# Kernel optimization log

Hardware: AMD Instinct MI355X
Metric: run time of the kernel (lower is better)

The kernel has to match this reference:

```python
import jax, jax.numpy as jnp
import numpy as np
from jax import lax

SEQ, FEAT, U1, U2, U3, OUT = 20, 5, 10, 7, 4, 4
BATCH = 262144


def _he_uniform(key, shape, fan_in):
    lim = np.sqrt(6.0 / fan_in)
    return jax.random.uniform(key, shape, jnp.float32, -lim, lim)


def _orthogonal(key, n, m):
    a = jax.random.normal(key, (max(n, m), min(n, m)), jnp.float32)
    q, _ = jnp.linalg.qr(a)
    return q[:n, :m] if n >= m else q[:m, :n].T


def _lstm_params(key, in_dim, units):
    k1, k2 = jax.random.split(key)
    Wk = _he_uniform(k1, (in_dim, 4 * units), in_dim)
    Wr = _orthogonal(k2, units, 4 * units)
    # Keras unit_forget_bias: bias = [zeros(i), ones(f), zeros(c), zeros(o)]
    b = jnp.concatenate([jnp.zeros(units), jnp.ones(units), jnp.zeros(2 * units)]).astype(jnp.float32)
    return Wk, Wr, b


def setup_inputs() -> dict:
    key = jax.random.key(0)
    ks = jax.random.split(key, 5)
    x = jax.random.normal(ks[0], (BATCH, SEQ, FEAT), jnp.float32)
    Wk1, Wr1, b1 = _lstm_params(ks[1], FEAT, U1)
    Wk2, Wr2, b2 = _lstm_params(ks[2], U1, U2)
    Wk3, Wr3, b3 = _lstm_params(ks[3], U2, U3)
    kd1, kd2 = jax.random.split(ks[4])
    lim = np.sqrt(6.0 / (U3 + OUT))  # glorot_uniform (Dense default)
    Wd = jax.random.uniform(kd1, (U3, OUT), jnp.float32, -lim, lim)
    bd = jnp.zeros((OUT,), jnp.float32)
    return {"x": x, "Wk1": Wk1, "Wr1": Wr1, "b1": b1,
            "Wk2": Wk2, "Wr2": Wr2, "b2": b2,
            "Wk3": Wk3, "Wr3": Wr3, "b3": b3,
            "Wd": Wd, "bd": bd}


def lstm_layer(x, Wk, Wr, b):
    # x: [B, T, F] -> h-sequence [B, T, U]; Keras gate order i, f, c(g), o
    B = x.shape[0]
    U = Wr.shape[0]
    # precompute input projection for all timesteps (one big GEMM)
    zx = jnp.einsum('btf,fg->btg', x, Wk) + b  # [B, T, 4U]
    zxT = jnp.swapaxes(zx, 0, 1)               # [T, B, 4U]

    def step(carry, zt):
        h, c = carry
        z = zt + h @ Wr
        i, f, g, o = jnp.split(z, 4, axis=-1)
        i = jax.nn.sigmoid(i)
        f = jax.nn.sigmoid(f)
        g = jnp.tanh(g)
        o = jax.nn.sigmoid(o)
        c = f * c + i * g
        h = o * jnp.tanh(c)
        return (h, c), h

    init = (jnp.zeros((B, U), x.dtype), jnp.zeros((B, U), x.dtype))
    _, hs = lax.scan(step, init, zxT)
    return jnp.swapaxes(hs, 0, 1)  # [B, T, U]


def reference(x, Wk1, Wr1, b1, Wk2, Wr2, b2, Wk3, Wr3, b3, Wd, bd):
    h = lstm_layer(x, Wk1, Wr1, b1)
    h = lstm_layer(h, Wk2, Wr2, b2)
    h = lstm_layer(h, Wk3, Wr3, b3)
    return jax.nn.sigmoid(jnp.einsum('btu,uo->bto', h, Wd) + bd)
```

## Files before the change

### kernel.cpp

```cpp
#include <hip/hip_runtime.h>

static constexpr int SEQ = 20, FEAT = 5, NU1 = 10, NU2 = 7, NU3 = 4, NOUT = 4;

typedef short bf16x8 __attribute__((ext_vector_type(8)));
typedef float f32x4  __attribute__((ext_vector_type(4)));


__device__ __forceinline__ unsigned short bf16_hi_rne(float x) {
    unsigned u = __float_as_uint(x);
    return (unsigned short)((u + 0x7FFF + ((u >> 16) & 1)) >> 16);
}
__device__ __forceinline__ unsigned short bf16_trunc(float x) {
    return (unsigned short)(__float_as_uint(x) >> 16);
}
__device__ __forceinline__ float bf16_to_f(unsigned short h) {
    return __uint_as_float(((unsigned)h) << 16);
}
__device__ __forceinline__ unsigned hpack(float h) {
    unsigned rp;
    asm("v_cvt_pk_bf16_f32 %0, %1, %1" : "=v"(rp) : "v"(h));
    float lo = h - __uint_as_float(rp << 16);
    return __builtin_amdgcn_perm(__float_as_uint(lo), rp, 0x07060100u);
}

__device__ __forceinline__ float sigm(float x) {
    return __builtin_amdgcn_rcpf(1.0f + __builtin_amdgcn_exp2f(x * -1.4426950408889634f));
}
__device__ __forceinline__ float ftanh(float x) {
    return 1.0f - 2.0f * __builtin_amdgcn_rcpf(1.0f + __builtin_amdgcn_exp2f(x * 2.8853900817779268f));
}

__device__ __forceinline__ unsigned act_unit(const f32x4 z, float& c) {
    float gi = sigm(z[0]), gf = sigm(z[1]), gg = ftanh(z[2]), go = sigm(z[3]);
    c = gf * c + gi * gg;
    return hpack(go * ftanh(c));
}

__device__ __forceinline__ unsigned bperm(int idx, unsigned v) {
    return (unsigned)__builtin_amdgcn_ds_bpermute(idx, (int)v);
}
__device__ __forceinline__ bf16x8 bfrag(unsigned v0, unsigned v1) {
    uint4 u{v0, v0, v1, v1};
    return __builtin_bit_cast(bf16x8, u);
}

__global__ void build_afrags(const float* Wk1, const float* Wr1, const float* b1,
                             const float* Wk2, const float* Wr2, const float* b2,
                             const float* Wk3, const float* Wr3, const float* b3,
                             const float* Wd,  const float* bd, unsigned* ws) {
    const int lane = threadIdx.x;
    const int m = lane & 15;
    const int qh = lane >> 4;

    for (int tau = 0; tau < 3; ++tau)
    for (int kap = 0; kap < 2; ++kap) {
        unsigned short h8[8];
        for (int j = 0; j < 8; ++j) {
            const int k = kap * 32 + qh * 8 + j;
            const int i = k >> 2, cls = k & 3;
            const int u = tau * 4 + (m >> 2), col = (m & 3) * NU1 + u;
            unsigned short v = 0;
            if (u < NU1) {
                if (i < 15) {
                    float W;
                    if (i < 8)       W = Wr1[((i >> 1) + 4 * (i & 1)) * 40 + col];
                    else if (i < 10) W = Wr1[i * 40 + col];
                    else             W = Wk1[(i - 10) * 40 + col];
                    unsigned short hi = bf16_hi_rne(W);
                    v = (cls < 2) ? hi : bf16_trunc(W - bf16_to_f(hi));
                } else if (i == 15) {
                    float bv = b1[col];
                    unsigned short hi = bf16_hi_rne(bv);
                    v = (cls == 0) ? hi : ((cls == 1) ? bf16_trunc(bv - bf16_to_f(hi)) : (unsigned short)0);
                }
            }
            h8[j] = v;
        }
        const int id = tau * 2 + kap;
        for (int d = 0; d < 4; ++d)
            ws[id * 256 + lane * 4 + d] = (unsigned)h8[2 * d] | ((unsigned)h8[2 * d + 1] << 16);
    }
    for (int tau = 0; tau < 2; ++tau)
    for (int kap = 0; kap < 3; ++kap) {
        unsigned short h8[8];
        for (int j = 0; j < 8; ++j) {
            const int k = kap * 32 + qh * 8 + j;
            const int i = k >> 2, cls = k & 3;
            const int u = tau * 4 + (m >> 2), col = (m & 3) * NU2 + u;
            unsigned short v = 0;
            if (u < NU2) {
                if (i < 17) {
                    float W;
                    if (i < 8)        W = Wk2[((i >> 1) + 4 * (i & 1)) * 28 + col];
                    else if (i < 10)  W = Wk2[i * 28 + col];
                    else if (i < 16)  W = Wr2[(((i - 10) >> 1) + 4 * ((i - 10) & 1)) * 28 + col];
                    else              W = Wr2[3 * 28 + col];
                    unsigned short hi = bf16_hi_rne(W);
                    v = (cls < 2) ? hi : bf16_trunc(W - bf16_to_f(hi));
                } else if (i == 17) {
                    float bv = b2[col];
                    unsigned short hi = bf16_hi_rne(bv);
                    v = (cls == 0) ? hi : ((cls == 1) ? bf16_trunc(bv - bf16_to_f(hi)) : (unsigned short)0);
                }
            }
            h8[j] = v;
        }
        const int id = 6 + tau * 3 + kap;
        for (int d = 0; d < 4; ++d)
            ws[id * 256 + lane * 4 + d] = (unsigned)h8[2 * d] | ((unsigned)h8[2 * d + 1] << 16);
    }
    for (int kap = 0; kap < 2; ++kap) {
        unsigned short h8[8];
        for (int j = 0; j < 8; ++j) {
            const int k = kap * 32 + qh * 8 + j;
            const int i = k >> 2, cls = k & 3;
            const int u = m >> 2, col = (m & 3) * NU3 + u;
            unsigned short v = 0;
            if (i < 11) {
                float W;
                if (i < 6)       W = Wk3[((i >> 1) + 4 * (i & 1)) * 16 + col];
                else if (i == 6) W = Wk3[3 * 16 + col];
                else             W = Wr3[(i - 7) * 16 + col];
                unsigned short hi = bf16_hi_rne(W);
                v = (cls < 2) ? hi : bf16_trunc(W - bf16_to_f(hi));
            } else if (i == 11) {
                float bv = b3[col];
                unsigned short hi = bf16_hi_rne(bv);
                v = (cls == 0) ? hi : ((cls == 1) ? bf16_trunc(bv - bf16_to_f(hi)) : (unsigned short)0);
            }
            h8[j] = v;
        }
        const int id = 12 + kap;
        for (int d = 0; d < 4; ++d)
            ws[id * 256 + lane * 4 + d] = (unsigned)h8[2 * d] | ((unsigned)h8[2 * d + 1] << 16);
    }
    {
        unsigned short h8[8];
        for (int j = 0; j < 8; ++j) {
            const int k = qh * 8 + j;
            const int i = k >> 2, cls = k & 3;
            unsigned short v = 0;
            if (m < NOUT) {
                if (i < 4) {
                    float W = Wd[i * NOUT + m];
                    unsigned short hi = bf16_hi_rne(W);
                    v = (cls < 2) ? hi : bf16_trunc(W - bf16_to_f(hi));
                } else if (i == 4) {
                    float bv = bd[m];
                    unsigned short hi = bf16_hi_rne(bv);
                    v = (cls == 0) ? hi : ((cls == 1) ? bf16_trunc(bv - bf16_to_f(hi)) : (unsigned short)0);
                }
            }
            h8[j] = v;
        }
        for (int d = 0; d < 4; ++d)
            ws[14 * 256 + lane * 4 + d] = (unsigned)h8[2 * d] | ((unsigned)h8[2 * d + 1] << 16);
    }
}

__global__ __launch_bounds__(256, 4) void lstm3_mfma(
    const float* __restrict__ x, const unsigned* __restrict__ wsA,
    float* __restrict__ out, int B) {
    const int tid = threadIdx.x;
    const int lane = tid & 63;
    const int n = lane & 15;
    const int q = lane >> 4;

    bf16x8 af[15];
#pragma unroll
    for (int i = 0; i < 15; ++i) {
        uint4 v = ((const uint4*)wsA)[i * 64 + lane];
        af[i] = __builtin_bit_cast(bf16x8, v);
    }

    const int i_h19 = (n + 16) << 2;
    const int i_sh  = (n + 16 * ((q + 3) & 3)) << 2;
    const int i_r1  = (n + 16 * ((q + 1) & 3)) << 2;
    const int i_r2  = (n + 16 * ((q + 2) & 3)) << 2;

    const unsigned ONE = 0x3F803F80u;
    const f32x4 zro = {0.f, 0.f, 0.f, 0.f};

    const int ngrp = B >> 4;
    const int gw = (blockIdx.x * blockDim.x + tid) >> 6;
    const int nw = (gridDim.x * blockDim.x) >> 6;

    for (int grp = gw; grp < ngrp; grp += nw) {
        const float* xr = x + (size_t)grp * 16 * (SEQ * FEAT) + n * (SEQ * FEAT);
        float* ob = out + (size_t)grp * 16 * (SEQ * NOUT) + n * (SEQ * NOUT);

        unsigned p1a = 0, p1b = 0, p1c = 0, t9 = 0;
        unsigned p2a = 0, p2b = 0, p3 = 0, rot = 0, rot2 = 0;
        float c10 = 0.f, c11 = 0.f, c12 = 0.f, c20 = 0.f, c21 = 0.f, c30 = 0.f;

        float xa = 0.f, xc = 0.f;
        if (q != 0) {
            const float* p = xr + 2 * (q - 1);
            xa = p[0];
            if (q != 3) xc = p[1];
        }

#pragma unroll 1
        for (int t = 0; t < SEQ; ++t) {
            const unsigned xP0 = hpack(xa), xP1 = hpack(xc);
            {
                const int tn = (t + 1 < SEQ) ? t + 1 : 0;
                if (q != 0) {
                    const float* p = xr + tn * FEAT + 2 * (q - 1);
                    xa = p[0];
                    if (q != 3) xc = p[1];
                }
            }
            bf16x8 bF0 = bfrag(p1a, p1b);
            unsigned F1v0 = (q == 0) ? p1c : xP0;
            unsigned F1v1 = (q == 0) ? t9 : ((q == 3) ? ONE : xP1);
            bf16x8 bF1 = bfrag(F1v0, F1v1);
            f32x4 z0 = __builtin_amdgcn_mfma_f32_16x16x32_bf16(af[0], bF0, zro, 0, 0, 0);
            z0 = __builtin_amdgcn_mfma_f32_16x16x32_bf16(af[1], bF1, z0, 0, 0, 0);
            f32x4 z1 = __builtin_amdgcn_mfma_f32_16x16x32_bf16(af[2], bF0, zro, 0, 0, 0);
            z1 = __builtin_amdgcn_mfma_f32_16x16x32_bf16(af[3], bF1, z1, 0, 0, 0);
            f32x4 z2 = __builtin_amdgcn_mfma_f32_16x16x32_bf16(af[4], bF0, zro, 0, 0, 0);
            z2 = __builtin_amdgcn_mfma_f32_16x16x32_bf16(af[5], bF1, z2, 0, 0, 0);
            const unsigned s2a = bperm(i_sh, p2a);
            const unsigned s2b = bperm(i_sh, p2b);
            p1a = act_unit(z0, c10);
            p1b = act_unit(z1, c11);
            p1c = act_unit(z2, c12);
            t9  = bperm(i_h19, p1c);
            bf16x8 bA  = bfrag(p1a, p1b);
            unsigned F2v0 = (q == 0) ? p1c : s2a;
            unsigned F2v1 = (q == 0) ? t9  : s2b;
            bf16x8 bF2 = bfrag(F2v0, F2v1);
            bf16x8 bF3 = bfrag(s2a, ONE);
            f32x4 y0 = __builtin_amdgcn_mfma_f32_16x16x32_bf16(af[6], bA, zro, 0, 0, 0);
            y0 = __builtin_amdgcn_mfma_f32_16x16x32_bf16(af[7], bF2, y0, 0, 0, 0);
            y0 = __builtin_amdgcn_mfma_f32_16x16x32_bf16(af[8], bF3, y0, 0, 0, 0);
            f32x4 y1 = __builtin_amdgcn_mfma_f32_16x16x32_bf16(af[9], bA, zro, 0, 0, 0);
            y1 = __builtin_amdgcn_mfma_f32_16x16x32_bf16(af[10], bF2, y1, 0, 0, 0);
            y1 = __builtin_amdgcn_mfma_f32_16x16x32_bf16(af[11], bF3, y1, 0, 0, 0);
            p2a = act_unit(y0, c20);
            p2b = act_unit(y1, c21);
            bf16x8 bF4 = bfrag(p2a, (q == 3) ? rot : p2b);
            unsigned F5v0 = (q == 0) ? rot  : rot2;
            unsigned F5v1 = (q == 0) ? rot2 : ONE;
            bf16x8 bF5 = bfrag(F5v0, F5v1);
            f32x4 w0 = __builtin_amdgcn_mfma_f32_16x16x32_bf16(af[12], bF4, zro, 0, 0, 0);
            w0 = __builtin_amdgcn_mfma_f32_16x16x32_bf16(af[13], bF5, w0, 0, 0, 0);
            p3 = act_unit(w0, c30);
            rot  = bperm(i_r1, p3);
            rot2 = bperm(i_r2, p3);
            unsigned F6v0 = (q == 0) ? p3 : ((q == 1) ? rot : ONE);
            unsigned F6v1 = (q == 0) ? rot : rot2;
            f32x4 o0 = __builtin_amdgcn_mfma_f32_16x16x32_bf16(af[14], bfrag(F6v0, F6v1), zro, 0, 0, 0);
            if (q == 0) {
                float4 o4;
                o4.x = sigm(o0[0]); o4.y = sigm(o0[1]);
                o4.z = sigm(o0[2]); o4.w = sigm(o0[3]);
                *(float4*)(ob + t * NOUT) = o4;
            }
        }
    }
}

extern "C" void kernel_launch(void* const* d_in, const int* in_sizes, int n_in,
                              void* d_out, int out_size, void* d_ws, size_t ws_size,
                              hipStream_t stream) {
    const float* x   = (const float*)d_in[0];
    const float* Wk1 = (const float*)d_in[1];
    const float* Wr1 = (const float*)d_in[2];
    const float* b1  = (const float*)d_in[3];
    const float* Wk2 = (const float*)d_in[4];
    const float* Wr2 = (const float*)d_in[5];
    const float* b2  = (const float*)d_in[6];
    const float* Wk3 = (const float*)d_in[7];
    const float* Wr3 = (const float*)d_in[8];
    const float* b3  = (const float*)d_in[9];
    const float* Wd  = (const float*)d_in[10];
    const float* bd  = (const float*)d_in[11];
    float* out = (float*)d_out;
    unsigned* ws = (unsigned*)d_ws;

    const int B = in_sizes[0] / (SEQ * FEAT);

    build_afrags<<<1, 64, 0, stream>>>(Wk1, Wr1, b1, Wk2, Wr2, b2,
                                       Wk3, Wr3, b3, Wd, bd, ws);
    lstm3_mfma<<<2048, 256, 0, stream>>>(x, ws, out, B);
}
```

Measured before the change: 386.2 us.

## Pack gate activations as float2, spread dense output over all lanes, double grid

Gate activation math now uses two-wide float vectors so the compiler can emit packed multiply and add instructions. The dense layer's A fragment now fills all 16 rows, so every quarter-wave holds a copy of the outputs. Each lane keeps one output value per timestep in registers and writes four sigmoid results every fourth step, which replaces the single-quarter float4 store and spreads the sigmoid work across all lanes. The grid is doubled to 4096 blocks, giving more resident waves or fewer grid-stride iterations per wave, at the cost of more register state per lane.

```diff
diff --git a/kernel.cpp b/kernel.cpp
--- a/kernel.cpp
+++ b/kernel.cpp
@@ -4,6 +4,9 @@
 
 typedef short bf16x8 __attribute__((ext_vector_type(8)));
 typedef float f32x4  __attribute__((ext_vector_type(4)));
+typedef float f32x2  __attribute__((ext_vector_type(2)));
+
+static constexpr unsigned ONE_P = 0x3F803F80u;
 
 
 __device__ __forceinline__ unsigned short bf16_hi_rne(float x) {
@@ -31,7 +34,20 @@
 }
 
 __device__ __forceinline__ unsigned act_unit(const f32x4 z, float& c) {
-    float gi = sigm(z[0]), gf = sigm(z[1]), gg = ftanh(z[2]), go = sigm(z[3]);
+    f32x2 a = {z[0], z[1]};
+    a = a * (-1.4426950408889634f);
+    f32x2 ea = {__builtin_amdgcn_exp2f(a[0]), __builtin_amdgcn_exp2f(a[1])};
+    ea = ea + 1.0f;
+    const float gi = __builtin_amdgcn_rcpf(ea[0]);
+    const float gf = __builtin_amdgcn_rcpf(ea[1]);
+    const f32x2 sc = {2.8853900817779268f, -1.4426950408889634f};
+    f32x2 b = {z[2], z[3]};
+    b = b * sc;
+    f32x2 eb = {__builtin_amdgcn_exp2f(b[0]), __builtin_amdgcn_exp2f(b[1])};
+    eb = eb + 1.0f;
+    const float rg = __builtin_amdgcn_rcpf(eb[0]);
+    const float go = __builtin_amdgcn_rcpf(eb[1]);
+    const float gg = 1.0f - 2.0f * rg;
     c = gf * c + gi * gg;
     return hpack(go * ftanh(c));
 }
@@ -42,6 +58,9 @@
 __device__ __forceinline__ bf16x8 bfrag(unsigned v0, unsigned v1) {
     uint4 u{v0, v0, v1, v1};
     return __builtin_bit_cast(bf16x8, u);
+}
+__device__ __forceinline__ f32x4 MF(bf16x8 a, bf16x8 b, f32x4 c) {
+    return __builtin_amdgcn_mfma_f32_16x16x32_bf16(a, b, c, 0, 0, 0);
 }
 
 __global__ void build_afrags(const float* Wk1, const float* Wr1, const float* b1,
@@ -140,16 +159,14 @@
             const int k = qh * 8 + j;
             const int i = k >> 2, cls = k & 3;
             unsigned short v = 0;
-            if (m < NOUT) {
-                if (i < 4) {
-                    float W = Wd[i * NOUT + m];
-                    unsigned short hi = bf16_hi_rne(W);
-                    v = (cls < 2) ? hi : bf16_trunc(W - bf16_to_f(hi));
-                } else if (i == 4) {
-                    float bv = bd[m];
-                    unsigned short hi = bf16_hi_rne(bv);
-                    v = (cls == 0) ? hi : ((cls == 1) ? bf16_trunc(bv - bf16_to_f(hi)) : (unsigned short)0);
-                }
+            if (i < 4) {
+                float W = Wd[i * NOUT + (m & 3)];
+                unsigned short hi = bf16_hi_rne(W);
+                v = (cls < 2) ? hi : bf16_trunc(W - bf16_to_f(hi));
+            } else if (i == 4) {
+                float bv = bd[m & 3];
+                unsigned short hi = bf16_hi_rne(bv);
+                v = (cls == 0) ? hi : ((cls == 1) ? bf16_trunc(bv - bf16_to_f(hi)) : (unsigned short)0);
             }
             h8[j] = v;
         }
@@ -178,7 +195,6 @@
     const int i_r1  = (n + 16 * ((q + 1) & 3)) << 2;
     const int i_r2  = (n + 16 * ((q + 2) & 3)) << 2;
 
-    const unsigned ONE = 0x3F803F80u;
     const f32x4 zro = {0.f, 0.f, 0.f, 0.f};
 
     const int ngrp = B >> 4;
@@ -192,6 +208,7 @@
         unsigned p1a = 0, p1b = 0, p1c = 0, t9 = 0;
         unsigned p2a = 0, p2b = 0, p3 = 0, rot = 0, rot2 = 0;
         float c10 = 0.f, c11 = 0.f, c12 = 0.f, c20 = 0.f, c21 = 0.f, c30 = 0.f;
+        float d0 = 0.f, d1 = 0.f, d2 = 0.f, d3 = 0.f;
 
         float xa = 0.f, xc = 0.f;
         if (q != 0) {
@@ -213,14 +230,11 @@
             }
             bf16x8 bF0 = bfrag(p1a, p1b);
             unsigned F1v0 = (q == 0) ? p1c : xP0;
-            unsigned F1v1 = (q == 0) ? t9 : ((q == 3) ? ONE : xP1);
+            unsigned F1v1 = (q == 0) ? t9 : ((q == 3) ? ONE_P : xP1);
             bf16x8 bF1 = bfrag(F1v0, F1v1);
-            f32x4 z0 = __builtin_amdgcn_mfma_f32_16x16x32_bf16(af[0], bF0, zro, 0, 0, 0);
-            z0 = __builtin_amdgcn_mfma_f32_16x16x32_bf16(af[1], bF1, z0, 0, 0, 0);
-            f32x4 z1 = __builtin_amdgcn_mfma_f32_16x16x32_bf16(af[2], bF0, zro, 0, 0, 0);
-            z1 = __builtin_amdgcn_mfma_f32_16x16x32_bf16(af[3], bF1, z1, 0, 0, 0);
-            f32x4 z2 = __builtin_amdgcn_mfma_f32_16x16x32_bf16(af[4], bF0, zro, 0, 0, 0);
-            z2 = __builtin_amdgcn_mfma_f32_16x16x32_bf16(af[5], bF1, z2, 0, 0, 0);
+            f32x4 z0 = MF(af[0], bF0, zro); z0 = MF(af[1], bF1, z0);
+            f32x4 z1 = MF(af[2], bF0, zro); z1 = MF(af[3], bF1, z1);
+            f32x4 z2 = MF(af[4], bF0, zro); z2 = MF(af[5], bF1, z2);
             const unsigned s2a = bperm(i_sh, p2a);
             const unsigned s2b = bperm(i_sh, p2b);
             p1a = act_unit(z0, c10);
@@ -231,32 +245,43 @@
             unsigned F2v0 = (q == 0) ? p1c : s2a;
             unsigned F2v1 = (q == 0) ? t9  : s2b;
             bf16x8 bF2 = bfrag(F2v0, F2v1);
-            bf16x8 bF3 = bfrag(s2a, ONE);
-            f32x4 y0 = __builtin_amdgcn_mfma_f32_16x16x32_bf16(af[6], bA, zro, 0, 0, 0);
-            y0 = __builtin_amdgcn_mfma_f32_16x16x32_bf16(af[7], bF2, y0, 0, 0, 0);
-            y0 = __builtin_amdgcn_mfma_f32_16x16x32_bf16(af[8], bF3, y0, 0, 0, 0);
-            f32x4 y1 = __builtin_amdgcn_mfma_f32_16x16x32_bf16(af[9], bA, zro, 0, 0, 0);
-            y1 = __builtin_amdgcn_mfma_f32_16x16x32_bf16(af[10], bF2, y1, 0, 0, 0);
-            y1 = __builtin_amdgcn_mfma_f32_16x16x32_bf16(af[11], bF3, y1, 0, 0, 0);
+            bf16x8 bF3 = bfrag(s2a, ONE_P);
+            f32x4 y0 = MF(af[6], bA, zro);
+            y0 = MF(af[7], bF2, y0);
+            y0 = MF(af[8], bF3, y0);
+            f32x4 y1 = MF(af[9], bA, zro);
+            y1 = MF(af[10], bF2, y1);
+            y1 = MF(af[11], bF3, y1);
             p2a = act_unit(y0, c20);
             p2b = act_unit(y1, c21);
             bf16x8 bF4 = bfrag(p2a, (q == 3) ? rot : p2b);
             unsigned F5v0 = (q == 0) ? rot  : rot2;
-            unsigned F5v1 = (q == 0) ? rot2 : ONE;
+            unsigned F5v1 = (q == 0) ? rot2 : ONE_P;
             bf16x8 bF5 = bfrag(F5v0, F5v1);
-            f32x4 w0 = __builtin_amdgcn_mfma_f32_16x16x32_bf16(af[12], bF4, zro, 0, 0, 0);
-            w0 = __builtin_amdgcn_mfma_f32_16x16x32_bf16(af[13], bF5, w0, 0, 0, 0);
+            f32x4 w0 = MF(af[12], bF4, zro);
+            w0 = MF(af[13], bF5, w0);
             p3 = act_unit(w0, c30);
             rot  = bperm(i_r1, p3);
             rot2 = bperm(i_r2, p3);
-            unsigned F6v0 = (q == 0) ? p3 : ((q == 1) ? rot : ONE);
+            unsigned F6v0 = (q == 0) ? p3 : ((q == 1) ? rot : ONE_P);
             unsigned F6v1 = (q == 0) ? rot : rot2;
-            f32x4 o0 = __builtin_amdgcn_mfma_f32_16x16x32_bf16(af[14], bfrag(F6v0, F6v1), zro, 0, 0, 0);
-            if (q == 0) {
-                float4 o4;
-                o4.x = sigm(o0[0]); o4.y = sigm(o0[1]);
-                o4.z = sigm(o0[2]); o4.w = sigm(o0[3]);
-                *(float4*)(ob + t * NOUT) = o4;
+            f32x4 o0 = MF(af[14], bfrag(F6v0, F6v1), zro);
+            {
+                float v01 = (q & 1) ? o0[1] : o0[0];
+                float v23 = (q & 1) ? o0[3] : o0[2];
+                float v = (q & 2) ? v23 : v01;
+                const int r = t & 3;
+                d0 = (r == 0) ? v : d0;
+                d1 = (r == 1) ? v : d1;
+                d2 = (r == 2) ? v : d2;
+                d3 = (r == 3) ? v : d3;
+            }
+            if ((t & 3) == 3) {
+                float* p = ob + (t - 3) * NOUT + q;
+                p[0 * NOUT] = sigm(d0);
+                p[1 * NOUT] = sigm(d1);
+                p[2 * NOUT] = sigm(d2);
+                p[3 * NOUT] = sigm(d3);
             }
         }
     }
@@ -284,5 +309,5 @@
 
     build_afrags<<<1, 64, 0, stream>>>(Wk1, Wr1, b1, Wk2, Wr2, b2,
                                        Wk3, Wr3, b3, Wd, bd, ws);
-    lstm3_mfma<<<2048, 256, 0, stream>>>(x, ws, out, B);
-}
+    lstm3_mfma<<<4096, 256, 0, stream>>>(x, ws, out, B);
+}
```

Result: no change. 378.6 us (-2.0%).
